# Performance work log

Hardware: AMD Instinct MI355X
Metric: run time of the kernel (lower is better)

Reference implementation:

```python
import jax, jax.numpy as jnp
import numpy as np

BEV_H = 150; BEV_W = 150; D = 4; NCAM = 6; C = 128
FH = 48; FW = 88            # camera feature map size
IMG_H = 480.0; IMG_W = 800.0  # raw image size used to normalize uv
PC = np.array([-51.2, -51.2, -5.0, 51.2, 51.2, 3.0], np.float32)  # pc_range


def setup_inputs() -> dict:
    key = jax.random.key(0)
    # GenerateGrid buffer: (D, 3, h, w) with channels (x, y, z), normalized to [0,1]
    z = PC[5] - PC[2]
    zs = (np.linspace(0.5, z - 0.5, D) / z).astype(np.float32)
    xs = (np.linspace(0.5, BEV_W - 0.5, BEV_W) / BEV_W).astype(np.float32)
    ys = (np.linspace(0.5, BEV_H - 0.5, BEV_H) / BEV_H).astype(np.float32)
    g = np.zeros((D, 3, BEV_H, BEV_W), np.float32)
    g[:, 0] = xs[None, None, :]
    g[:, 1] = ys[None, :, None]
    g[:, 2] = zs[:, None, None]
    # realistic surround-camera rig: 6 cams looking outward every 60 deg
    I = np.zeros((1, NCAM, 3, 3), np.float32)
    E = np.zeros((1, NCAM, 4, 4), np.float32)
    for i in range(NCAM):
        I[0, i] = [[500.0, 0.0, 400.0], [0.0, 500.0, 240.0], [0.0, 0.0, 1.0]]
        yaw = 2.0 * np.pi * i / NCAM
        fwd = np.array([np.cos(yaw), np.sin(yaw), 0.0])
        right = np.array([np.sin(yaw), -np.cos(yaw), 0.0])
        down = np.array([0.0, 0.0, -1.0])
        R = np.stack([right, down, fwd])  # rows = camera axes in ego frame
        campos = np.array([1.5 * np.cos(yaw), 1.5 * np.sin(yaw), 1.5])
        E[0, i, :3, :3] = R
        E[0, i, :3, 3] = -R @ campos
        E[0, i, 3, 3] = 1.0
    feat = jax.random.normal(key, (1, NCAM, FH, FW, C), jnp.float32)
    return {"feat": feat, "I": jnp.asarray(I), "E": jnp.asarray(E), "grid_3d": jnp.asarray(g)}


def _forward(feat, I, E, grid_3d):
    b, n = I.shape[:2]
    d, _, h, w = grid_3d.shape
    Q = h * w
    scale = jnp.asarray([PC[3] - PC[0], PC[4] - PC[1], PC[5] - PC[2]], feat.dtype)
    off = jnp.asarray([PC[0], PC[1], PC[2]], feat.dtype)
    # (D, Q, 3) ego-frame 3D reference points, then homogeneous (D, Q, 4)
    rp = grid_3d.reshape(d, 3, Q).transpose(0, 2, 1) * scale + off
    rp4 = jnp.concatenate([rp, jnp.ones((d, Q, 1), rp.dtype)], axis=-1)
    # lidar2img = I @ E[:, :, :3, :] -> (b, n, 3, 4); project -> (b, n, D, Q, 3)
    l2i = jnp.einsum('bnij,bnjk->bnik', I, E[:, :, :3, :])
    proj = jnp.einsum('bnij,dqj->bndqi', l2i, rp4)
    eps = 1e-5
    zc = proj[..., 2]
    mask = zc > eps
    uv = proj[..., :2] / jnp.maximum(zc, eps)[..., None]
    u = uv[..., 0] / IMG_W
    v = uv[..., 1] / IMG_H
    mask = mask & (u > 0.0) & (u < 1.0) & (v > 0.0) & (v < 1.0)
    # bilinear grid_sample (align_corners=False, zero padding) at (u, v)
    px = u * FW - 0.5
    py = v * FH - 0.5
    x0 = jnp.floor(px)
    y0 = jnp.floor(py)
    wx1 = px - x0; wy1 = py - y0
    wx0 = 1.0 - wx1; wy0 = 1.0 - wy1
    x0i = x0.astype(jnp.int32)
    y0i = y0.astype(jnp.int32)
    ff = feat.reshape(b, n, FH * FW, C)

    def gather(xi, yi, wt):
        valid = (xi >= 0) & (xi < FW) & (yi >= 0) & (yi < FH)
        idx = (jnp.clip(yi, 0, FH - 1) * FW + jnp.clip(xi, 0, FW - 1)).reshape(b, n, d * Q)
        g = jnp.take_along_axis(ff, idx[..., None], axis=2).reshape(b, n, d, Q, C)
        return g * (wt * valid.astype(feat.dtype))[..., None]

    sampled = (gather(x0i, y0i, wx0 * wy0) + gather(x0i + 1, y0i, wx1 * wy0)
               + gather(x0i, y0i + 1, wx0 * wy1) + gather(x0i + 1, y0i + 1, wx1 * wy1))
    # mask-weighted fusion over cameras and pillar points (BEVFormer SCA)
    m = mask.astype(feat.dtype)
    out = jnp.einsum('bndq,bndqc->bqc', m, sampled)
    cnt = jnp.clip(m.sum(axis=(1, 2)), 1.0, None)
    return out / cnt[..., None]  # (b, Q, C)


def reference(feat, I, E, grid_3d):
    return _forward(feat, I, E, grid_3d)
```

## Files before the change

### kernel.cpp

```cpp
#include <hip/hip_runtime.h>

#define BEV_H 150
#define BEV_W 150
#define NCAM  6
#define CC    128
#define FH    48
#define FW    88
#define IMG_Hf 480.0f
#define IMG_Wf 800.0f
#define NPTS  24

__device__ __forceinline__ float rdlanef(float x, int l) {
    return __uint_as_float((unsigned)__builtin_amdgcn_readlane((int)__float_as_uint(x), l));
}

__global__ __launch_bounds__(128, 8) void bev_sample_kernel(
    const float* __restrict__ feat,
    const float* __restrict__ I_,
    const float* __restrict__ E_,
    const float* __restrict__ grid,
    float* __restrict__ out)
{
    const int tid  = threadIdx.x;
    const int lane = tid & 63;
    const int wv   = tid >> 6;
    const int l32  = lane & 31;
    const bool lowhalf = (lane < 32);

    const int r    = blockIdx.x & 7;
    const int i    = blockIdx.x >> 3;
    const int row0 = (r < 4) ? 0 : 38;
    const int nrow = (r < 4) ? 38 : 37;
    const int c3   = r & 3;
    const int col0 = c3 * 19;
    const int wr   = (c3 == 3) ? 18 : 19;
    if (i >= nrow * wr) return;
    int ph, pw;
    if (wr == 19) { ph = i / 19; pw = i - ph * 19; }
    else          { ph = i / 18; pw = i - ph * 18; }
    ph += row0; pw += col0;

    const int h  = ph * 2 + wv;
    const int wA = pw * 2;
    const int qA = h * BEV_W + wA;

    const bool actA = (lane < NPTS);
    const bool actB = (lane >= 32) && (lane < 32 + NPTS);
    float gx = 0.f, gy = 0.f, gz = 0.f;
    int n = 0;
    if (actA || actB) {
        n = l32 >> 2;
        const int d = l32 & 3;
        const int wc = wA + (actB ? 1 : 0);
        gx = grid[((d * 3 + 0) * BEV_H + h) * BEV_W + wc];
        gy = grid[((d * 3 + 1) * BEV_H + h) * BEV_W + wc];
        gz = grid[((d * 3 + 2) * BEV_H + h) * BEV_W + wc];
    }

    __shared__ __align__(16) float s_l2i[NCAM][12];
    if (tid < NCAM * 12) {
        const int nn = tid / 12, rr = tid % 12;
        const int ii = rr >> 2, j = rr & 3;
        float acc = 0.f;
        #pragma unroll
        for (int k = 0; k < 3; ++k)
            acc += I_[nn * 9 + ii * 3 + k] * E_[nn * 16 + k * 4 + j];
        s_l2i[nn][rr] = acc;
    }
    __syncthreads();

    int   iT = 0, iB = 0;
    float wTL = 0.f, wTR = 0.f, wBL = 0.f, wBR = 0.f;
    bool  m = false;

    if (actA || actB) {
        const float x = gx * 102.4f - 51.2f;
        const float y = gy * 102.4f - 51.2f;
        const float z = gz * 8.0f   - 5.0f;

        const float4 M0 = *(const float4*)&s_l2i[n][0];
        const float4 M1 = *(const float4*)&s_l2i[n][4];
        const float4 M2 = *(const float4*)&s_l2i[n][8];
        const float p0 = M0.x * x + M0.y * y + M0.z * z + M0.w;
        const float p1 = M1.x * x + M1.y * y + M1.z * z + M1.w;
        const float p2 = M2.x * x + M2.y * y + M2.z * z + M2.w;

        const float eps = 1e-5f;
        const float zc = fmaxf(p2, eps);
        const float u = (p0 / zc) * (1.0f / IMG_Wf);
        const float v = (p1 / zc) * (1.0f / IMG_Hf);
        m = (p2 > eps) && (u > 0.f) && (u < 1.f) && (v > 0.f) && (v < 1.f);

        const float px = u * (float)FW - 0.5f;
        const float py = v * (float)FH - 0.5f;
        const float fx0 = floorf(px), fy0 = floorf(py);
        const int x0 = (int)fx0, y0 = (int)fy0;
        const int x1 = x0 + 1,   y1 = y0 + 1;
        const float wx1 = px - fx0, wy1 = py - fy0;
        const float wx0 = 1.f - wx1, wy0 = 1.f - wy1;

        const bool vx0 = (x0 >= 0) && (x0 < FW);
        const bool vx1 = (x1 >= 0) && (x1 < FW);
        const bool vy0 = (y0 >= 0) && (y0 < FH);
        const bool vy1 = (y1 >= 0) && (y1 < FH);
        const int cx0 = min(max(x0, 0), FW - 1), cx1 = min(max(x1, 0), FW - 1);
        const int cy0 = min(max(y0, 0), FH - 1), cy1 = min(max(y1, 0), FH - 1);

        const float w0v = wx0 * wy0 * ((vx0 && vy0) ? 1.f : 0.f);
        const float w1v = wx1 * wy0 * ((vx1 && vy0) ? 1.f : 0.f);
        const float w2v = wx0 * wy1 * ((vx0 && vy1) ? 1.f : 0.f);
        const float w3v = wx1 * wy1 * ((vx1 && vy1) ? 1.f : 0.f);

        const int bx = min(max(x0, 0), FW - 2);
        wTL = ((cx0 == bx)     ? w0v : 0.f) + ((cx1 == bx)     ? w1v : 0.f);
        wTR = ((cx0 == bx + 1) ? w0v : 0.f) + ((cx1 == bx + 1) ? w1v : 0.f);
        wBL = ((cx0 == bx)     ? w2v : 0.f) + ((cx1 == bx)     ? w3v : 0.f);
        wBR = ((cx0 == bx + 1) ? w2v : 0.f) + ((cx1 == bx + 1) ? w3v : 0.f);

        const int base = n * FH * FW;
        iT = (base + cy0 * FW + bx) * CC;
        iB = (base + cy1 * FW + bx) * CC;
    }

    const unsigned long long bal = __ballot(m);
    unsigned balA = (unsigned)(bal & 0xFFFFFFull);
    unsigned balB = (unsigned)((bal >> 32) & 0xFFFFFFull);
    const float cntA = fmaxf((float)__popc(balA), 1.f);
    const float cntB = fmaxf((float)__popc(balB), 1.f);

    float aAx = 0.f, aAy = 0.f, aAz = 0.f, aAw = 0.f;
    float aBx = 0.f, aBy = 0.f, aBz = 0.f, aBw = 0.f;
    const int loff = 4 * lane;

    while (balA | balB) {
        int eA = 0, eB = 32;
        float sA = 0.f, sB = 0.f;
        if (balA) { eA = __builtin_ctz(balA); balA &= balA - 1; sA = 1.f; }
        if (balB) { eB = 32 + __builtin_ctz(balB); balB &= balB - 1; sB = 1.f; }

        const int jTA = __builtin_amdgcn_readlane(iT, eA);
        const int jBA = __builtin_amdgcn_readlane(iB, eA);
        const int jTB = __builtin_amdgcn_readlane(iT, eB);
        const int jBB = __builtin_amdgcn_readlane(iB, eB);

        const float4 fTA = *(const float4*)(feat + jTA + loff);
        const float4 fBA = *(const float4*)(feat + jBA + loff);
        const float4 fTB = *(const float4*)(feat + jTB + loff);
        const float4 fBB = *(const float4*)(feat + jBB + loff);

        const float wTA = sA * (lowhalf ? rdlanef(wTL, eA) : rdlanef(wTR, eA));
        const float wBA = sA * (lowhalf ? rdlanef(wBL, eA) : rdlanef(wBR, eA));
        const float wTB = sB * (lowhalf ? rdlanef(wTL, eB) : rdlanef(wTR, eB));
        const float wBB = sB * (lowhalf ? rdlanef(wBL, eB) : rdlanef(wBR, eB));

        aAx += wTA * fTA.x + wBA * fBA.x;
        aAy += wTA * fTA.y + wBA * fBA.y;
        aAz += wTA * fTA.z + wBA * fBA.z;
        aAw += wTA * fTA.w + wBA * fBA.w;
        aBx += wTB * fTB.x + wBB * fBB.x;
        aBy += wTB * fTB.y + wBB * fBB.y;
        aBz += wTB * fTB.z + wBB * fBB.z;
        aBw += wTB * fTB.w + wBB * fBB.w;
    }

    aAx += __shfl_xor(aAx, 32);  aAy += __shfl_xor(aAy, 32);
    aAz += __shfl_xor(aAz, 32);  aAw += __shfl_xor(aAw, 32);
    aBx += __shfl_xor(aBx, 32);  aBy += __shfl_xor(aBy, 32);
    aBz += __shfl_xor(aBz, 32);  aBw += __shfl_xor(aBw, 32);

    const float inv = lowhalf ? (1.f / cntA) : (1.f / cntB);
    const int   q   = lowhalf ? qA : (qA + 1);
    float4 o;
    o.x = (lowhalf ? aAx : aBx) * inv;
    o.y = (lowhalf ? aAy : aBy) * inv;
    o.z = (lowhalf ? aAz : aBz) * inv;
    o.w = (lowhalf ? aAw : aBw) * inv;
    *(float4*)(out + q * CC + 4 * l32) = o;
}

extern "C" void kernel_launch(void* const* d_in, const int* in_sizes, int n_in,
                              void* d_out, int out_size, void* d_ws, size_t ws_size,
                              hipStream_t stream) {
    const float* feat = (const float*)d_in[0];
    const float* I_   = (const float*)d_in[1];
    const float* E_   = (const float*)d_in[2];
    const float* grid = (const float*)d_in[3];
    float* out        = (float*)d_out;

    bev_sample_kernel<<<8 * 722, 128, 0, stream>>>(feat, I_, E_, grid, out);
}
```

Measured before the change: 18.75 us.

## Repack features into bf16 2x2 patch layout and gather one block per sample

Adds a prepass kernel that converts the camera feature map to bf16 and stores it as overlapping 2x2 pixel patches (256 channels-entries per patch) in the workspace. The sampling kernel then fetches each valid sample's whole bilinear neighbourhood with a single 16-byte load per lane and processes one ballot bit per iteration instead of two. This halves gathered bytes and the number of scattered loads. In exchange it adds an extra kernel launch that reads the full fp32 features and writes a roughly 2x-duplicated bf16 copy every call, and it reduces feature precision to bf16.

```diff
diff --git a/kernel.cpp b/kernel.cpp
--- a/kernel.cpp
+++ b/kernel.cpp
@@ -9,13 +9,54 @@
 #define IMG_Hf 480.0f
 #define IMG_Wf 800.0f
 #define NPTS  24
+#define YB    (FH - 1)
 
 __device__ __forceinline__ float rdlanef(float x, int l) {
     return __uint_as_float((unsigned)__builtin_amdgcn_readlane((int)__float_as_uint(x), l));
 }
+__device__ __forceinline__ float bflo(unsigned x) { return __uint_as_float(x << 16); }
+__device__ __forceinline__ float bfhi(unsigned x) { return __uint_as_float(x & 0xffff0000u); }
+
+#define NBLK (NCAM * YB * FW)
+#define NTHR (NBLK * 32)
+
+__global__ __launch_bounds__(256) void repack_kernel(
+    const float* __restrict__ feat, unsigned short* __restrict__ pack)
+{
+    const int t = blockIdx.x * 256 + threadIdx.x;
+    if (t >= NTHR) return;
+    const int blk = t >> 5;
+    const int sub = t & 31;
+    const int cam = blk / (YB * FW);
+    const int rem = blk - cam * (YB * FW);
+    const int yb  = rem / FW;
+    const int x   = rem - yb * FW;
+    const int row = yb + (sub >> 4);
+    const int ch  = (sub & 15) * 8;
+
+    const float4* src = (const float4*)(feat + ((cam * FH + row) * FW + x) * CC + ch);
+    const float4 v0 = src[0];
+    const float4 v1 = src[1];
+    unsigned a = __float_as_uint(v0.x), b = __float_as_uint(v0.y);
+    unsigned c = __float_as_uint(v0.z), d = __float_as_uint(v0.w);
+    unsigned e = __float_as_uint(v1.x), f = __float_as_uint(v1.y);
+    unsigned g = __float_as_uint(v1.z), h2 = __float_as_uint(v1.w);
+    a = (a + 0x7fffu + ((a >> 16) & 1u)) >> 16;
+    b = (b + 0x7fffu + ((b >> 16) & 1u)) >> 16;
+    c = (c + 0x7fffu + ((c >> 16) & 1u)) >> 16;
+    d = (d + 0x7fffu + ((d >> 16) & 1u)) >> 16;
+    e = (e + 0x7fffu + ((e >> 16) & 1u)) >> 16;
+    f = (f + 0x7fffu + ((f >> 16) & 1u)) >> 16;
+    g = (g + 0x7fffu + ((g >> 16) & 1u)) >> 16;
+    h2 = (h2 + 0x7fffu + ((h2 >> 16) & 1u)) >> 16;
+    uint4 o;
+    o.x = a | (b << 16); o.y = c | (d << 16);
+    o.z = e | (f << 16); o.w = g | (h2 << 16);
+    *(uint4*)(pack + blk * 256 + sub * 8) = o;
+}
 
 __global__ __launch_bounds__(128, 8) void bev_sample_kernel(
-    const float* __restrict__ feat,
+    const unsigned short* __restrict__ pack,
     const float* __restrict__ I_,
     const float* __restrict__ E_,
     const float* __restrict__ grid,
@@ -25,7 +66,6 @@
     const int lane = tid & 63;
     const int wv   = tid >> 6;
     const int l32  = lane & 31;
-    const bool lowhalf = (lane < 32);
 
     const int r    = blockIdx.x & 7;
     const int i    = blockIdx.x >> 3;
@@ -69,8 +109,8 @@
     }
     __syncthreads();
 
-    int   iT = 0, iB = 0;
-    float wTL = 0.f, wTR = 0.f, wBL = 0.f, wBR = 0.f;
+    int   iP = 0;
+    float wP00 = 0.f, wP01 = 0.f, wP10 = 0.f, wP11 = 0.f;
     bool  m = false;
 
     if (actA || actB) {
@@ -112,70 +152,94 @@
         const float w3v = wx1 * wy1 * ((vx1 && vy1) ? 1.f : 0.f);
 
         const int bx = min(max(x0, 0), FW - 2);
-        wTL = ((cx0 == bx)     ? w0v : 0.f) + ((cx1 == bx)     ? w1v : 0.f);
-        wTR = ((cx0 == bx + 1) ? w0v : 0.f) + ((cx1 == bx + 1) ? w1v : 0.f);
-        wBL = ((cx0 == bx)     ? w2v : 0.f) + ((cx1 == bx)     ? w3v : 0.f);
-        wBR = ((cx0 == bx + 1) ? w2v : 0.f) + ((cx1 == bx + 1) ? w3v : 0.f);
-
-        const int base = n * FH * FW;
-        iT = (base + cy0 * FW + bx) * CC;
-        iB = (base + cy1 * FW + bx) * CC;
-    }
-
-    const unsigned long long bal = __ballot(m);
-    unsigned balA = (unsigned)(bal & 0xFFFFFFull);
-    unsigned balB = (unsigned)((bal >> 32) & 0xFFFFFFull);
-    const float cntA = fmaxf((float)__popc(balA), 1.f);
-    const float cntB = fmaxf((float)__popc(balB), 1.f);
-
-    float aAx = 0.f, aAy = 0.f, aAz = 0.f, aAw = 0.f;
-    float aBx = 0.f, aBy = 0.f, aBz = 0.f, aBw = 0.f;
-    const int loff = 4 * lane;
-
-    while (balA | balB) {
-        int eA = 0, eB = 32;
-        float sA = 0.f, sB = 0.f;
-        if (balA) { eA = __builtin_ctz(balA); balA &= balA - 1; sA = 1.f; }
-        if (balB) { eB = 32 + __builtin_ctz(balB); balB &= balB - 1; sB = 1.f; }
-
-        const int jTA = __builtin_amdgcn_readlane(iT, eA);
-        const int jBA = __builtin_amdgcn_readlane(iB, eA);
-        const int jTB = __builtin_amdgcn_readlane(iT, eB);
-        const int jBB = __builtin_amdgcn_readlane(iB, eB);
-
-        const float4 fTA = *(const float4*)(feat + jTA + loff);
-        const float4 fBA = *(const float4*)(feat + jBA + loff);
-        const float4 fTB = *(const float4*)(feat + jTB + loff);
-        const float4 fBB = *(const float4*)(feat + jBB + loff);
-
-        const float wTA = sA * (lowhalf ? rdlanef(wTL, eA) : rdlanef(wTR, eA));
-        const float wBA = sA * (lowhalf ? rdlanef(wBL, eA) : rdlanef(wBR, eA));
-        const float wTB = sB * (lowhalf ? rdlanef(wTL, eB) : rdlanef(wTR, eB));
-        const float wBB = sB * (lowhalf ? rdlanef(wBL, eB) : rdlanef(wBR, eB));
-
-        aAx += wTA * fTA.x + wBA * fBA.x;
-        aAy += wTA * fTA.y + wBA * fBA.y;
-        aAz += wTA * fTA.z + wBA * fBA.z;
-        aAw += wTA * fTA.w + wBA * fBA.w;
-        aBx += wTB * fTB.x + wBB * fBB.x;
-        aBy += wTB * fTB.y + wBB * fBB.y;
-        aBz += wTB * fTB.z + wBB * fBB.z;
-        aBw += wTB * fTB.w + wBB * fBB.w;
-    }
-
-    aAx += __shfl_xor(aAx, 32);  aAy += __shfl_xor(aAy, 32);
-    aAz += __shfl_xor(aAz, 32);  aAw += __shfl_xor(aAw, 32);
-    aBx += __shfl_xor(aBx, 32);  aBy += __shfl_xor(aBy, 32);
-    aBz += __shfl_xor(aBz, 32);  aBw += __shfl_xor(aBw, 32);
-
-    const float inv = lowhalf ? (1.f / cntA) : (1.f / cntB);
-    const int   q   = lowhalf ? qA : (qA + 1);
-    float4 o;
-    o.x = (lowhalf ? aAx : aBx) * inv;
-    o.y = (lowhalf ? aAy : aBy) * inv;
-    o.z = (lowhalf ? aAz : aBz) * inv;
-    o.w = (lowhalf ? aAw : aBw) * inv;
-    *(float4*)(out + q * CC + 4 * l32) = o;
+        const int yb = min(max(y0, 0), FH - 2);
+
+        const float cA0 = (cx0 == bx)     ? 1.f : 0.f;
+        const float cA1 = (cx1 == bx)     ? 1.f : 0.f;
+        const float cB0 = (cx0 == bx + 1) ? 1.f : 0.f;
+        const float cB1 = (cx1 == bx + 1) ? 1.f : 0.f;
+        const float tL = w0v * cA0 + w1v * cA1;
+        const float tR = w0v * cB0 + w1v * cB1;
+        const float bL = w2v * cA0 + w3v * cA1;
+        const float bR = w2v * cB0 + w3v * cB1;
+
+        const float rT0 = (cy0 == yb)     ? 1.f : 0.f;
+        const float rT1 = (cy1 == yb)     ? 1.f : 0.f;
+        const float rB0 = (cy0 == yb + 1) ? 1.f : 0.f;
+        const float rB1 = (cy1 == yb + 1) ? 1.f : 0.f;
+
+        wP00 = tL * rT0 + bL * rT1;
+        wP01 = tL * rB0 + bL * rB1;
+        wP10 = tR * rT0 + bR * rT1;
+        wP11 = tR * rB0 + bR * rB1;
+
+        iP = ((n * YB + yb) * FW + bx) * 256;
+    }
+
+    unsigned long long bal = __ballot(m);
+    const float cntA = fmaxf((float)__popcll(bal & 0xFFFFFFull), 1.f);
+    const float cntB = fmaxf((float)__popcll((bal >> 32) & 0xFFFFFFull), 1.f);
+
+    float aA[8] = {0.f, 0.f, 0.f, 0.f, 0.f, 0.f, 0.f, 0.f};
+    float aB[8] = {0.f, 0.f, 0.f, 0.f, 0.f, 0.f, 0.f, 0.f};
+    const int loff = 8 * lane;
+    const bool hi16 = (lane & 16) != 0;
+    const bool hi32 = (lane & 32) != 0;
+
+    while (bal) {
+        const int e = (int)__builtin_ctzll(bal);
+        bal &= bal - 1;
+
+        const int j = __builtin_amdgcn_readlane(iP, e) + loff;
+        const uint4 d = *(const uint4*)(pack + j);
+
+        const float w00 = rdlanef(wP00, e);
+        const float w01 = rdlanef(wP01, e);
+        const float w10 = rdlanef(wP10, e);
+        const float w11 = rdlanef(wP11, e);
+        const float wlo = hi16 ? w01 : w00;
+        const float whi = hi16 ? w11 : w10;
+        const float w   = hi32 ? whi : wlo;
+
+        const float v0 = bflo(d.x), v1 = bfhi(d.x);
+        const float v2 = bflo(d.y), v3 = bfhi(d.y);
+        const float v4 = bflo(d.z), v5 = bfhi(d.z);
+        const float v6 = bflo(d.w), v7 = bfhi(d.w);
+
+        if (e < 32) {
+            aA[0] += w * v0; aA[1] += w * v1; aA[2] += w * v2; aA[3] += w * v3;
+            aA[4] += w * v4; aA[5] += w * v5; aA[6] += w * v6; aA[7] += w * v7;
+        } else {
+            aB[0] += w * v0; aB[1] += w * v1; aB[2] += w * v2; aB[3] += w * v3;
+            aB[4] += w * v4; aB[5] += w * v5; aB[6] += w * v6; aB[7] += w * v7;
+        }
+    }
+
+    #pragma unroll
+    for (int c = 0; c < 8; ++c) {
+        aA[c] += __shfl_xor(aA[c], 16);
+        aA[c] += __shfl_xor(aA[c], 32);
+        aB[c] += __shfl_xor(aB[c], 16);
+        aB[c] += __shfl_xor(aB[c], 32);
+    }
+
+    if (lane < 32) {
+        const bool isA = (lane < 16);
+        const float inv = isA ? (1.f / cntA) : (1.f / cntB);
+        const int   q   = isA ? qA : (qA + 1);
+        const int   ch  = (lane & 15) * 8;
+        float4 o0, o1;
+        if (isA) {
+            o0.x = aA[0] * inv; o0.y = aA[1] * inv; o0.z = aA[2] * inv; o0.w = aA[3] * inv;
+            o1.x = aA[4] * inv; o1.y = aA[5] * inv; o1.z = aA[6] * inv; o1.w = aA[7] * inv;
+        } else {
+            o0.x = aB[0] * inv; o0.y = aB[1] * inv; o0.z = aB[2] * inv; o0.w = aB[3] * inv;
+            o1.x = aB[4] * inv; o1.y = aB[5] * inv; o1.z = aB[6] * inv; o1.w = aB[7] * inv;
+        }
+        float4* dst = (float4*)(out + q * CC + ch);
+        dst[0] = o0;
+        dst[1] = o1;
+    }
 }
 
 extern "C" void kernel_launch(void* const* d_in, const int* in_sizes, int n_in,
@@ -187,5 +251,7 @@
     const float* grid = (const float*)d_in[3];
     float* out        = (float*)d_out;
 
-    bev_sample_kernel<<<8 * 722, 128, 0, stream>>>(feat, I_, E_, grid, out);
-}
+    unsigned short* pack = (unsigned short*)d_ws;
+    repack_kernel<<<(NTHR + 255) / 256, 256, 0, stream>>>(feat, pack);
+    bev_sample_kernel<<<8 * 722, 128, 0, stream>>>(pack, I_, E_, grid, out);
+}
```

Result: slower. 28.62 us (+52.6%).
